# Optimization experiments

Hardware: AMD Instinct MI355X
Metric: run time of the kernel (lower is better)

The kernel has to match this reference:

```python
import jax, jax.numpy as jnp
import numpy as np
from jax import lax
import math

KS = 7  # attention kernel size
PAD = 3


def conv2d(x, w, b, pad):
    y = lax.conv_general_dilated(x, w, (1, 1), [(pad, pad), (pad, pad)],
                                 dimension_numbers=('NCHW', 'OIHW', 'NCHW'))
    return y + b[None, :, None, None]


def unfold(x):
    # x: [B, C, H, W] -> [B, C, KS*KS, H, W], matching nn.Unfold channel-major order
    B, C, H, W = x.shape
    xp = jnp.pad(x, ((0, 0), (0, 0), (PAD, PAD), (PAD, PAD)))
    patches = [xp[:, :, i:i + H, j:j + W] for i in range(KS) for j in range(KS)]
    return jnp.stack(patches, axis=2)


def setup_inputs() -> dict:
    key = jax.random.key(0)
    ks = jax.random.split(key, 12)
    B, H, W = 1, 256, 256
    s = lambda fan: 1.0 / np.sqrt(fan)
    inp = {
        'x': jax.random.normal(ks[0], (B, 6, H, W), jnp.float32),
        'w0': jax.random.normal(ks[1], (48, 3, 3, 3), jnp.float32) * s(3 * 9),
        'b0': jnp.zeros((48,), jnp.float32),
        'w1': jax.random.normal(ks[2], (48, 48, 3, 3), jnp.float32) * s(48 * 9),
        'b1': jnp.zeros((48,), jnp.float32),
        'w2': jax.random.normal(ks[3], (48, 48, 3, 3), jnp.float32) * s(48 * 9),
        'b2': jnp.zeros((48,), jnp.float32),
        'w3': jax.random.normal(ks[4], (24, 48, 3, 3), jnp.float32) * s(48 * 9),
        'b3': jnp.zeros((24,), jnp.float32),
        'skip_w': jax.random.normal(ks[5], (24, 3, 1, 1), jnp.float32) * s(3),
        'skip_b': jnp.zeros((24,), jnp.float32),
        'q_w': jax.random.normal(ks[6], (24, 24, 1, 1), jnp.float32) * s(24),
        'q_b': jnp.zeros((24,), jnp.float32),
        'k_w': jax.random.normal(ks[7], (24, 24, 1, 1), jnp.float32) * s(24),
        'k_b': jnp.zeros((24,), jnp.float32),
        'v_w': jax.random.normal(ks[8], (24, 24, 1, 1), jnp.float32) * s(24),
        'v_b': jnp.zeros((24,), jnp.float32),
    }
    return inp


def reference(x, w0, b0, w1, b1, w2, b2, w3, b3, skip_w, skip_b,
              q_w, q_b, k_w, k_b, v_w, v_b):
    def submodel(t):
        h = jax.nn.relu(conv2d(t, w0, b0, 1))
        h = jax.nn.relu(conv2d(h, w1, b1, 1))
        h = jax.nn.relu(conv2d(h, w2, b2, 1))
        h = jax.nn.relu(conv2d(h, w3, b3, 1))
        return h + conv2d(t, skip_w, skip_b, 0)

    xa, xb = jnp.split(x, 2, axis=1)  # [B,3,H,W] each
    a = submodel(xa)                  # [B,24,H,W]
    b = submodel(xb)

    Q = conv2d(b, q_w, q_b, 0)        # [B,24,H,W]
    K = unfold(conv2d(a, k_w, k_b, 0))  # [B,24,49,H,W]
    V = unfold(conv2d(a, v_w, v_b, 0))  # [B,24,49,H,W]

    C = Q.shape[1]
    A = jnp.einsum('bchw,bcphw->bphw', Q, K) / math.sqrt(C)
    A = jax.nn.softmax(A, axis=1)     # softmax over 49 local positions
    y = jnp.einsum('bphw,bcphw->bchw', A, V)
    return jnp.concatenate([y + a, b], axis=1)  # [B,48,H,W]
```

## Files before the change

kernel.cpp:

```cpp
#include <hip/hip_runtime.h>
#include <math.h>

#define HH 256
#define WW 256
#define NN (HH * WW)

typedef _Float16 f16;
typedef _Float16 f16x8 __attribute__((ext_vector_type(8)));
typedef _Float16 f16x4 __attribute__((ext_vector_type(4)));
typedef float f32x4 __attribute__((ext_vector_type(4)));

#define OQ 75264

__global__ __launch_bounds__(256) void prep_kernel(
    const float* __restrict__ x, const float* __restrict__ w0,
    const float* __restrict__ w1, const float* __restrict__ w2,
    const float* __restrict__ w3, const float* __restrict__ qw,
    const float* __restrict__ kw, const float* __restrict__ vw,
    f16* __restrict__ xh, f16* __restrict__ bf) {
  if (blockIdx.x < 512) {
    int p = blockIdx.x * 256 + threadIdx.x;
    int z = p >= NN;
    int q = p - z * NN;
    const float* xz = x + (size_t)z * 3 * NN;
    f16x4 v;
    v[0] = (f16)xz[q];
    v[1] = (f16)xz[NN + q];
    v[2] = (f16)xz[2 * NN + q];
    v[3] = (f16)0.f;
    *(f16x4*)(xh + (size_t)p * 4) = v;
    return;
  }
  const int O1 = 1536, O2 = O1 + 27648, O3 = O2 + 27648;
  int e = (blockIdx.x - 512) * 256 + threadIdx.x;
  if (e >= OQ + 3072) return;
  float val = 0.f;
  if (e >= OQ) {
    int idx = e - OQ;
    int mat = idx >> 10;
    int r = idx & 1023;
    int nt = r >> 9;
    int lane = (r >> 3) & 63;
    int j = r & 7;
    int n = lane & 15, quad = lane >> 4;
    int ci = quad * 8 + j, co = nt * 16 + n;
    const float* w = (mat == 0) ? qw : (mat == 1) ? kw : vw;
    if (ci < 24 && co < 24) val = w[co * 24 + ci];
  } else if (e < O1) {
    int idx = e;
    int j = idx & 7;
    int lane = (idx >> 3) & 63;
    int nt = idx >> 9;
    int n = lane & 15, quad = lane >> 4;
    int k = quad * 8 + j;
    int cout = nt * 16 + n;
    if (k < 27) {
      int tap = k / 3, ci = k - tap * 3;
      val = w0[(cout * 3 + ci) * 9 + tap];
    }
  } else {
    const float* w;
    int COUT, idx;
    if (e < O2)      { w = w1; COUT = 48; idx = e - O1; }
    else if (e < O3) { w = w2; COUT = 48; idx = e - O2; }
    else             { w = w3; COUT = 24; idx = e - O3; }
    const int NT = (COUT == 48) ? 3 : 2;
    int j = idx & 7;
    int lane = (idx >> 3) & 63;
    int rest = idx >> 9;
    int nt = rest % NT;
    int q2 = rest / NT;
    int kc = q2 & 1;
    int tap = q2 >> 1;
    int n = lane & 15, quad = lane >> 4;
    int ci = kc * 32 + quad * 8 + j;
    int cout = nt * 16 + n;
    if (ci < 48 && cout < COUT) val = w[(cout * 48 + ci) * 9 + tap];
  }
  bf[e] = (f16)val;
}

__global__ __launch_bounds__(256, 2) void conv0_gemm(
    const f16* __restrict__ xh, const f16* __restrict__ bf0,
    const float* __restrict__ bias, f16* __restrict__ outh) {
  extern __shared__ char smem[];
  const int tid = threadIdx.x;
  const int lane = tid & 63, wave = tid >> 6;
  const int n = lane & 15, quad = lane >> 4;
  const int bx = blockIdx.x * 16, by = blockIdx.y * 16, z = blockIdx.z;
  const f16* xz = xh + (size_t)z * NN * 4;

  {
    int p = tid, y = p >> 4, xcol = p & 15;
    int gy = by + y, gx = bx + xcol;
    f16* row = (f16*)(smem + p * 80);
#pragma unroll
    for (int tap = 0; tap < 9; ++tap) {
      int dy = tap / 3, dx = tap - (tap / 3) * 3;
      int sy = gy + dy - 1, sx = gx + dx - 1;
      f16 c0 = (f16)0.f, c1 = c0, c2 = c0;
      if (sy >= 0 && sy < HH && sx >= 0 && sx < WW) {
        const f16* s = xz + ((size_t)sy * WW + sx) * 4;
        c0 = s[0]; c1 = s[1]; c2 = s[2];
      }
      row[tap * 3 + 0] = c0;
      row[tap * 3 + 1] = c1;
      row[tap * 3 + 2] = c2;
    }
#pragma unroll
    for (int k = 27; k < 32; ++k) row[k] = (f16)0.f;
  }
  __syncthreads();

  f32x4 acc[4][3];
#pragma unroll
  for (int nt = 0; nt < 3; ++nt) {
    float bv = bias[nt * 16 + n];
#pragma unroll
    for (int i = 0; i < 4; ++i) acc[i][nt] = (f32x4){bv, bv, bv, bv};
  }
  f16x8 B[3];
#pragma unroll
  for (int nt = 0; nt < 3; ++nt)
    B[nt] = *(const f16x8*)(bf0 + (nt * 64 + lane) * 8);
#pragma unroll
  for (int i = 0; i < 4; ++i) {
    int r = wave * 4 + i;
    f16x8 a = *(const f16x8*)(smem + (r * 16 + n) * 80 + quad * 16);
#pragma unroll
    for (int nt = 0; nt < 3; ++nt)
      acc[i][nt] =
          __builtin_amdgcn_mfma_f32_16x16x32_f16(a, B[nt], acc[i][nt], 0, 0, 0);
  }

  f16* oz = outh + (size_t)z * NN * 48;
#pragma unroll
  for (int i = 0; i < 4; ++i) {
    int y = by + wave * 4 + i;
#pragma unroll
    for (int nt = 0; nt < 3; ++nt)
#pragma unroll
      for (int reg = 0; reg < 4; ++reg)
        oz[((size_t)y * WW + bx + quad * 4 + reg) * 48 + nt * 16 + n] =
            (f16)fmaxf(acc[i][nt][reg], 0.f);
  }
}

template <int NT, int COUT, bool FUSE>
__global__ __launch_bounds__(256, 4) void gemm_conv(
    const f16* __restrict__ in, const f16* __restrict__ bfr,
    const float* __restrict__ bias, f16* __restrict__ outh,
    const float* __restrict__ xsrc, const float* __restrict__ skw,
    const float* __restrict__ skb) {
  extern __shared__ char smem[];
  float* xt = (float*)(smem + 180 * 144);
  const int tid = threadIdx.x;
  const int lane = tid & 63, wave = tid >> 6;
  const int n = lane & 15, quad = lane >> 4;
  const int bx = blockIdx.x * 16, by = blockIdx.y * 8, z = blockIdx.z;
  const f16* inz = in + (size_t)z * NN * 48;

  if (tid < 180) {
    int p = tid;
    int yy = p / 18, xx = p - yy * 18;
    int gy = by + yy - 1, gx = bx + xx - 1;
    float4* dst = (float4*)(smem + p * 144);
    if (gy >= 0 && gy < HH && gx >= 0 && gx < WW) {
      const float4* s = (const float4*)(inz + ((size_t)gy * WW + gx) * 48);
      float4 a0 = s[0], a1 = s[1], a2 = s[2], a3 = s[3], a4 = s[4], a5 = s[5];
      dst[0] = a0; dst[1] = a1; dst[2] = a2;
      dst[3] = a3; dst[4] = a4; dst[5] = a5;
      dst[6] = make_float4(0, 0, 0, 0);
      dst[7] = make_float4(0, 0, 0, 0);
    } else {
      float4 zz = make_float4(0, 0, 0, 0);
#pragma unroll
      for (int c = 0; c < 8; ++c) dst[c] = zz;
    }
  }
  if (FUSE) {
    for (int i = tid; i < 384; i += 256) {
      int c = i >> 7, p = i & 127;
      xt[i] = xsrc[(size_t)z * 3 * NN + c * NN + (by + (p >> 4)) * WW + bx +
                   (p & 15)];
    }
  }
  __syncthreads();

  f32x4 acc[2][NT];
#pragma unroll
  for (int nt = 0; nt < NT; ++nt) {
    int cc = nt * 16 + n;
    float bv = (cc < COUT) ? bias[cc] : 0.f;
#pragma unroll
    for (int i = 0; i < 2; ++i) acc[i][nt] = (f32x4){bv, bv, bv, bv};
  }

  const int r0 = wave * 2;
#pragma unroll 1
  for (int tap = 0; tap < 9; ++tap) {
    const int dy = tap / 3, dx = tap - dy * 3;
    f16x8 B[2][NT];
#pragma unroll
    for (int kc = 0; kc < 2; ++kc)
#pragma unroll
      for (int nt = 0; nt < NT; ++nt)
        B[kc][nt] = *(const f16x8*)(bfr +
                                    (((tap * 2 + kc) * NT + nt) * 64 + lane) * 8);
#pragma unroll
    for (int i = 0; i < 2; ++i) {
      const int p = (r0 + i + dy) * 18 + (n + dx);
      const char* ap = smem + p * 144;
      f16x8 a0 = *(const f16x8*)(ap + quad * 16);
      f16x8 a1 = *(const f16x8*)(ap + 64 + quad * 16);
#pragma unroll
      for (int nt = 0; nt < NT; ++nt)
        acc[i][nt] = __builtin_amdgcn_mfma_f32_16x16x32_f16(a0, B[0][nt],
                                                            acc[i][nt], 0, 0, 0);
#pragma unroll
      for (int nt = 0; nt < NT; ++nt)
        acc[i][nt] = __builtin_amdgcn_mfma_f32_16x16x32_f16(a1, B[1][nt],
                                                            acc[i][nt], 0, 0, 0);
    }
  }

  if (!FUSE) {
    f16* oz = outh + (size_t)z * NN * 48;
#pragma unroll
    for (int i = 0; i < 2; ++i) {
      int y = by + r0 + i;
#pragma unroll
      for (int nt = 0; nt < NT; ++nt)
#pragma unroll
        for (int reg = 0; reg < 4; ++reg)
          oz[((size_t)y * WW + bx + quad * 4 + reg) * 48 + nt * 16 + n] =
              (f16)fmaxf(acc[i][nt][reg], 0.f);
    }
  } else {
    f16* oz = outh + (size_t)z * NN * 32;
#pragma unroll
    for (int i = 0; i < 2; ++i) {
      int y = by + r0 + i;
#pragma unroll
      for (int nt = 0; nt < NT; ++nt) {
        int cc = nt * 16 + n;
        float s0 = 0.f, s1 = 0.f, s2 = 0.f, sb0 = 0.f;
        if (cc < 24) {
          s0 = skw[cc * 3 + 0];
          s1 = skw[cc * 3 + 1];
          s2 = skw[cc * 3 + 2];
          sb0 = skb[cc];
        }
#pragma unroll
        for (int reg = 0; reg < 4; ++reg) {
          float v = 0.f;
          if (cc < 24) {
            int pl = (r0 + i) * 16 + quad * 4 + reg;
            float sk = sb0 + s0 * xt[pl] + s1 * xt[128 + pl] + s2 * xt[256 + pl];
            v = fmaxf(acc[i][nt][reg], 0.f) + sk;
          }
          oz[((size_t)(y * WW + bx + quad * 4 + reg)) * 32 + cc] = (f16)v;
        }
      }
    }
  }
}

__global__ __launch_bounds__(256) void q_mfma(const f16* __restrict__ ABh,
                                              const f16* __restrict__ bf,
                                              const float* __restrict__ qb,
                                              f16* __restrict__ Qh) {
  const int tid = threadIdx.x;
  const int lane = tid & 63, wave = tid >> 6;
  const int n = lane & 15, quad = lane >> 4;
  const f16* src = ABh + (size_t)NN * 32;
  f16x8 QF[2];
#pragma unroll
  for (int nt = 0; nt < 2; ++nt)
    QF[nt] = *(const f16x8*)(bf + OQ + (nt * 64 + lane) * 8);
  float qbias[2];
#pragma unroll
  for (int nt = 0; nt < 2; ++nt) {
    int cc = nt * 16 + n;
    qbias[nt] = (cc < 24) ? qb[cc] : 0.f;
  }
#pragma unroll
  for (int t = 0; t < 4; ++t) {
    int T = blockIdx.x * 16 + wave * 4 + t;
    size_t p0 = (size_t)T * 16;
    f16x8 a8 = *(const f16x8*)(src + p0 * 32 + n * 32 + quad * 8);
#pragma unroll
    for (int nt = 0; nt < 2; ++nt) {
      f32x4 acc = {qbias[nt], qbias[nt], qbias[nt], qbias[nt]};
      acc = __builtin_amdgcn_mfma_f32_16x16x32_f16(a8, QF[nt], acc, 0, 0, 0);
      int cc = nt * 16 + n;
      if (cc < 24) {
#pragma unroll
        for (int reg = 0; reg < 4; ++reg)
          Qh[(p0 + quad * 4 + reg) * 24 + cc] = (f16)acc[reg];
      }
    }
  }
}

__device__ inline float dot8p(f16x8 a, f16x8 b, float acc) {
#if __has_builtin(__builtin_amdgcn_fdot2)
  acc = __builtin_amdgcn_fdot2(__builtin_shufflevector(a, a, 0, 1),
                               __builtin_shufflevector(b, b, 0, 1), acc, false);
  acc = __builtin_amdgcn_fdot2(__builtin_shufflevector(a, a, 2, 3),
                               __builtin_shufflevector(b, b, 2, 3), acc, false);
  acc = __builtin_amdgcn_fdot2(__builtin_shufflevector(a, a, 4, 5),
                               __builtin_shufflevector(b, b, 4, 5), acc, false);
  acc = __builtin_amdgcn_fdot2(__builtin_shufflevector(a, a, 6, 7),
                               __builtin_shufflevector(b, b, 6, 7), acc, false);
  return acc;
#else
#pragma unroll
  for (int i = 0; i < 8; ++i) acc += (float)a[i] * (float)b[i];
  return acc;
#endif
}

__global__ __launch_bounds__(256, 3) void attn_kernel(
    const f16* __restrict__ Qh, const f16* __restrict__ ABh,
    const f16* __restrict__ bf, const float* __restrict__ kb,
    const float* __restrict__ vb, float* __restrict__ out) {
  extern __shared__ f16 kv[];
  const int tid = threadIdx.x;
  const int lane = tid & 63, wave = tid >> 6;
  const int n16 = lane & 15, quad = lane >> 4;
  const int bx = blockIdx.x * 32, by = blockIdx.y * 8;
  const int xl = tid & 31, yl = tid >> 5;
  const int p = (by + yl) * WW + bx + xl;
  const f16* ah = ABh;
  const f16* bh = ABh + (size_t)NN * 32;

  f16x8 q0 = *(const f16x8*)(Qh + (size_t)p * 24);
  f16x8 q1 = *(const f16x8*)(Qh + (size_t)p * 24 + 8);
  f16x8 q2 = *(const f16x8*)(Qh + (size_t)p * 24 + 16);

  for (int idx = tid; idx < 2128; idx += 256) {
    int row = idx / 152;
    int rem = idx - row * 152;
    int pxl = rem >> 2;
    int c = rem & 3;
    int gy = by + row - 3, gx = bx + pxl - 3;
    f16x8 v = {};
    if (gy >= 0 && gy < HH && gx >= 0 && gx < WW)
      v = *(const f16x8*)(ah + ((size_t)(gy * WW + gx)) * 32 + c * 8);
    *(f16x8*)(kv + (row * 38 + pxl) * 56 + c * 8) = v;
  }
  __syncthreads();

  const f16* cs = kv + ((yl + 3) * 38 + xl + 3) * 56;
  f16x8 a0 = *(const f16x8*)(cs);
  f16x8 a1 = *(const f16x8*)(cs + 8);
  f16x8 a2 = *(const f16x8*)(cs + 16);
  __syncthreads();

  {
    f16x8 KF[2], VF[2];
#pragma unroll
    for (int nt = 0; nt < 2; ++nt) {
      KF[nt] = *(const f16x8*)(bf + OQ + 1024 + (nt * 64 + lane) * 8);
      VF[nt] = *(const f16x8*)(bf + OQ + 2048 + (nt * 64 + lane) * 8);
    }
    float kbias[2], vbias[2];
#pragma unroll
    for (int nt = 0; nt < 2; ++nt) {
      int cc = nt * 16 + n16;
      kbias[nt] = (cc < 24) ? kb[cc] : 0.f;
      vbias[nt] = (cc < 24) ? vb[cc] : 0.f;
    }
    for (int t = wave; t < 34; t += 4) {
      f16x8 a8 = *(const f16x8*)(kv + (t * 16 + n16) * 56 + quad * 8);
#pragma unroll
      for (int nt = 0; nt < 2; ++nt) {
        f32x4 ak = {kbias[nt], kbias[nt], kbias[nt], kbias[nt]};
        f32x4 av = {vbias[nt], vbias[nt], vbias[nt], vbias[nt]};
        ak = __builtin_amdgcn_mfma_f32_16x16x32_f16(a8, KF[nt], ak, 0, 0, 0);
        av = __builtin_amdgcn_mfma_f32_16x16x32_f16(a8, VF[nt], av, 0, 0, 0);
        int cc = nt * 16 + n16;
        if (cc < 24) {
#pragma unroll
          for (int reg = 0; reg < 4; ++reg) {
            f16* slot = kv + (t * 16 + quad * 4 + reg) * 56;
            slot[cc] = (f16)ak[reg];
            slot[24 + cc] = (f16)av[reg];
          }
        }
      }
    }
  }
  __syncthreads();

  float s[49];
#pragma unroll
  for (int pp = 0; pp < 49; ++pp) {
    int dy = pp / 7, dx = pp - dy * 7;
    const f16* base = kv + ((yl + dy) * 38 + xl + dx) * 56;
    f16x8 k0 = *(const f16x8*)(base);
    f16x8 k1 = *(const f16x8*)(base + 8);
    f16x8 k2 = *(const f16x8*)(base + 16);
    float d = 0.f;
    d = dot8p(q0, k0, d);
    d = dot8p(q1, k1, d);
    d = dot8p(q2, k2, d);
    s[pp] = d * 0.20412414523193154f;
  }

  float m = s[0];
#pragma unroll
  for (int pp = 1; pp < 49; ++pp) m = fmaxf(m, s[pp]);
  float den = 0.f;
#pragma unroll
  for (int pp = 0; pp < 49; ++pp) {
    float e = __expf(s[pp] - m);
    s[pp] = e;
    den += e;
  }
  const float inv = 1.f / den;

  f16x8 y0 = {}, y1 = {}, y2 = {};
#pragma unroll
  for (int pp = 0; pp < 49; ++pp) {
    int dy = pp / 7, dx = pp - dy * 7;
    const f16* base = kv + ((yl + dy) * 38 + xl + dx) * 56 + 24;
    f16 wh = (f16)(s[pp] * inv);
    f16x8 w8 = {wh, wh, wh, wh, wh, wh, wh, wh};
    f16x8 v0 = *(const f16x8*)(base);
    f16x8 v1 = *(const f16x8*)(base + 8);
    f16x8 v2 = *(const f16x8*)(base + 16);
    y0 = v0 * w8 + y0;
    y1 = v1 * w8 + y1;
    y2 = v2 * w8 + y2;
  }

  f16x8 b0 = *(const f16x8*)(bh + (size_t)p * 32);
  f16x8 b1 = *(const f16x8*)(bh + (size_t)p * 32 + 8);
  f16x8 b2 = *(const f16x8*)(bh + (size_t)p * 32 + 16);
#pragma unroll
  for (int c = 0; c < 8; ++c) {
    out[(size_t)c * NN + p] = (float)y0[c] + (float)a0[c];
    out[(size_t)(8 + c) * NN + p] = (float)y1[c] + (float)a1[c];
    out[(size_t)(16 + c) * NN + p] = (float)y2[c] + (float)a2[c];
    out[(size_t)(24 + c) * NN + p] = (float)b0[c];
    out[(size_t)(32 + c) * NN + p] = (float)b1[c];
    out[(size_t)(40 + c) * NN + p] = (float)b2[c];
  }
}

extern "C" void kernel_launch(void* const* d_in, const int* in_sizes, int n_in,
                              void* d_out, int out_size, void* d_ws,
                              size_t ws_size, hipStream_t stream) {
  const float* x = (const float*)d_in[0];
  const float* w0 = (const float*)d_in[1];
  const float* b0 = (const float*)d_in[2];
  const float* w1 = (const float*)d_in[3];
  const float* b1 = (const float*)d_in[4];
  const float* w2 = (const float*)d_in[5];
  const float* b2 = (const float*)d_in[6];
  const float* w3 = (const float*)d_in[7];
  const float* b3 = (const float*)d_in[8];
  const float* sw = (const float*)d_in[9];
  const float* sb = (const float*)d_in[10];
  const float* qw = (const float*)d_in[11];
  const float* qb = (const float*)d_in[12];
  const float* kw = (const float*)d_in[13];
  const float* kb = (const float*)d_in[14];
  const float* vw = (const float*)d_in[15];
  const float* vb = (const float*)d_in[16];
  float* out = (float*)d_out;
  float* ws = (float*)d_ws;

  f16* Qh = (f16*)(ws);
  f16* ABh = (f16*)(ws + (size_t)12 * NN);
  f16* ACT0 = (f16*)(ws + (size_t)44 * NN);
  f16* ACT1 = (f16*)(ws + (size_t)92 * NN);
  f16* XH = (f16*)(ws + (size_t)140 * NN);
  f16* BF = (f16*)(ws + (size_t)144 * NN);

  prep_kernel<<<dim3(818), dim3(256), 0, stream>>>(x, w0, w1, w2, w3, qw, kw,
                                                   vw, XH, BF);

  conv0_gemm<<<dim3(16, 16, 2), dim3(256), 256 * 80, stream>>>(XH, BF, b0,
                                                               ACT0);
  dim3 g2(16, 32, 2);
  gemm_conv<3, 48, false><<<g2, dim3(256), 180 * 144, stream>>>(
      ACT0, BF + 1536, b1, ACT1, nullptr, nullptr, nullptr);
  gemm_conv<3, 48, false><<<g2, dim3(256), 180 * 144, stream>>>(
      ACT1, BF + 29184, b2, ACT0, nullptr, nullptr, nullptr);
  gemm_conv<2, 24, true><<<g2, dim3(256), 180 * 144 + 1536, stream>>>(
      ACT0, BF + 56832, b3, ABh, x, sw, sb);

  q_mfma<<<dim3(256), dim3(256), 0, stream>>>(ABh, BF, qb, Qh);

  attn_kernel<<<dim3(8, 32), dim3(256), 544 * 112, stream>>>(Qh, ABh, BF, kb,
                                                             vb, out);
}
```

Before: 158.8 us.

## Fuse whole pipeline into one cooperative persistent kernel with grid syncs

Replaces the seven separate kernel launches with a single cooperative kernel of 512 blocks that runs weight repacking, the four conv layers, Q projection and local attention as phases separated by grid-wide syncs. Conv0 now reads fp32 input directly, which drops the separate fp16 input conversion pass. The attention phase computes K/V projections per tile in shared memory and splits the 49 neighbours across two thread halves, merging them with an online-softmax combine. The aim is to remove launch gaps and inter-kernel idle time. The cost is fixed grid size, grid.sync overhead, and a smaller attention tile that recomputes K/V over a larger halo, which may lower per-phase efficiency.

Measured after the change: 480.6 us. 203% more time.

```diff
diff --git a/kernel.cpp b/kernel.cpp
--- a/kernel.cpp
+++ b/kernel.cpp
@@ -1,16 +1,486 @@
 #include <hip/hip_runtime.h>
+#include <hip/hip_cooperative_groups.h>
 #include <math.h>
+
+namespace cg = cooperative_groups;
 
 #define HH 256
 #define WW 256
 #define NN (HH * WW)
 
 typedef _Float16 f16;
+typedef _Float16 f16x4 __attribute__((ext_vector_type(4)));
 typedef _Float16 f16x8 __attribute__((ext_vector_type(8)));
-typedef _Float16 f16x4 __attribute__((ext_vector_type(4)));
 typedef float f32x4 __attribute__((ext_vector_type(4)));
 
 #define OQ 75264
+
+__device__ inline float dot8p(f16x8 a, f16x8 b, float acc) {
+#if __has_builtin(__builtin_amdgcn_fdot2)
+  acc = __builtin_amdgcn_fdot2(__builtin_shufflevector(a, a, 0, 1),
+                               __builtin_shufflevector(b, b, 0, 1), acc, false);
+  acc = __builtin_amdgcn_fdot2(__builtin_shufflevector(a, a, 2, 3),
+                               __builtin_shufflevector(b, b, 2, 3), acc, false);
+  acc = __builtin_amdgcn_fdot2(__builtin_shufflevector(a, a, 4, 5),
+                               __builtin_shufflevector(b, b, 4, 5), acc, false);
+  acc = __builtin_amdgcn_fdot2(__builtin_shufflevector(a, a, 6, 7),
+                               __builtin_shufflevector(b, b, 6, 7), acc, false);
+  return acc;
+#else
+#pragma unroll
+  for (int i = 0; i < 8; ++i) acc += (float)a[i] * (float)b[i];
+  return acc;
+#endif
+}
+
+__device__ __forceinline__ float repack_elem(
+    int e, const float* __restrict__ w0, const float* __restrict__ w1,
+    const float* __restrict__ w2, const float* __restrict__ w3,
+    const float* __restrict__ qw, const float* __restrict__ kw,
+    const float* __restrict__ vw) {
+  const int O1 = 1536, O2 = O1 + 27648, O3 = O2 + 27648;
+  float val = 0.f;
+  if (e >= OQ) {
+    int idx = e - OQ;
+    int mat = idx >> 10;
+    int r = idx & 1023;
+    int nt = r >> 9;
+    int ln = (r >> 3) & 63;
+    int j = r & 7;
+    int nn = ln & 15, qd = ln >> 4;
+    int ci = qd * 8 + j, co = nt * 16 + nn;
+    const float* w = (mat == 0) ? qw : (mat == 1) ? kw : vw;
+    if (ci < 24 && co < 24) val = w[co * 24 + ci];
+  } else if (e < O1) {
+    int j = e & 7;
+    int ln = (e >> 3) & 63;
+    int nt = e >> 9;
+    int nn = ln & 15, qd = ln >> 4;
+    int k = qd * 8 + j;
+    int cout = nt * 16 + nn;
+    if (k < 27) {
+      int tap = k / 3, ci = k - tap * 3;
+      val = w0[(cout * 3 + ci) * 9 + tap];
+    }
+  } else {
+    const float* w;
+    int COUT, idx;
+    if (e < O2)      { w = w1; COUT = 48; idx = e - O1; }
+    else if (e < O3) { w = w2; COUT = 48; idx = e - O2; }
+    else             { w = w3; COUT = 24; idx = e - O3; }
+    const int NT = (COUT == 48) ? 3 : 2;
+    int j = idx & 7;
+    int ln = (idx >> 3) & 63;
+    int rest = idx >> 9;
+    int nt = rest % NT;
+    int q2 = rest / NT;
+    int kc = q2 & 1;
+    int tap = q2 >> 1;
+    int nn = ln & 15, qd = ln >> 4;
+    int ci = kc * 32 + qd * 8 + j;
+    int cout = nt * 16 + nn;
+    if (ci < 48 && cout < COUT) val = w[(cout * 48 + ci) * 9 + tap];
+  }
+  return val;
+}
+
+template <int NT, int COUT, bool FUSE>
+__device__ __forceinline__ void conv_layer(
+    const f16* __restrict__ in, const f16* __restrict__ bfr,
+    const float* __restrict__ bias, f16* __restrict__ outh,
+    const float* __restrict__ xsrc, const float* __restrict__ skw,
+    const float* __restrict__ skb, char* smem, int tid, int bx, int by,
+    int z) {
+  float* xt = (float*)(smem + 180 * 144);
+  const int lane = tid & 63, wave = tid >> 6;
+  const int n = lane & 15, quad = lane >> 4;
+  const f16* inz = in + (size_t)z * NN * 48;
+
+  if (tid < 180) {
+    int p = tid;
+    int yy = p / 18, xx = p - yy * 18;
+    int gy = by + yy - 1, gx = bx + xx - 1;
+    float4* dst = (float4*)(smem + p * 144);
+    if (gy >= 0 && gy < HH && gx >= 0 && gx < WW) {
+      const float4* s = (const float4*)(inz + ((size_t)gy * WW + gx) * 48);
+      float4 a0 = s[0], a1 = s[1], a2 = s[2], a3 = s[3], a4 = s[4], a5 = s[5];
+      dst[0] = a0; dst[1] = a1; dst[2] = a2;
+      dst[3] = a3; dst[4] = a4; dst[5] = a5;
+      dst[6] = make_float4(0, 0, 0, 0);
+      dst[7] = make_float4(0, 0, 0, 0);
+    } else {
+      float4 zz = make_float4(0, 0, 0, 0);
+#pragma unroll
+      for (int c = 0; c < 8; ++c) dst[c] = zz;
+    }
+  }
+  if (FUSE) {
+    for (int i = tid; i < 384; i += 256) {
+      int c = i >> 7, p = i & 127;
+      xt[i] = xsrc[(size_t)z * 3 * NN + c * NN + (by + (p >> 4)) * WW + bx +
+                   (p & 15)];
+    }
+  }
+  __syncthreads();
+
+  f32x4 acc[2][NT];
+#pragma unroll
+  for (int nt = 0; nt < NT; ++nt) {
+    int cc = nt * 16 + n;
+    float bv = (cc < COUT) ? bias[cc] : 0.f;
+#pragma unroll
+    for (int i = 0; i < 2; ++i) acc[i][nt] = (f32x4){bv, bv, bv, bv};
+  }
+
+  const int r0 = wave * 2;
+#pragma unroll 1
+  for (int tap = 0; tap < 9; ++tap) {
+    const int dy = tap / 3, dx = tap - dy * 3;
+    f16x8 B[2][NT];
+#pragma unroll
+    for (int kc = 0; kc < 2; ++kc)
+#pragma unroll
+      for (int nt = 0; nt < NT; ++nt)
+        B[kc][nt] = *(const f16x8*)(bfr +
+                                    (((tap * 2 + kc) * NT + nt) * 64 + lane) * 8);
+#pragma unroll
+    for (int i = 0; i < 2; ++i) {
+      const int p = (r0 + i + dy) * 18 + (n + dx);
+      const char* ap = smem + p * 144;
+      f16x8 a0 = *(const f16x8*)(ap + quad * 16);
+      f16x8 a1 = *(const f16x8*)(ap + 64 + quad * 16);
+#pragma unroll
+      for (int nt = 0; nt < NT; ++nt)
+        acc[i][nt] = __builtin_amdgcn_mfma_f32_16x16x32_f16(a0, B[0][nt],
+                                                            acc[i][nt], 0, 0, 0);
+#pragma unroll
+      for (int nt = 0; nt < NT; ++nt)
+        acc[i][nt] = __builtin_amdgcn_mfma_f32_16x16x32_f16(a1, B[1][nt],
+                                                            acc[i][nt], 0, 0, 0);
+    }
+  }
+
+  if (!FUSE) {
+    f16* oz = outh + (size_t)z * NN * 48;
+#pragma unroll
+    for (int i = 0; i < 2; ++i) {
+      int y = by + r0 + i;
+#pragma unroll
+      for (int nt = 0; nt < NT; ++nt)
+#pragma unroll
+        for (int reg = 0; reg < 4; ++reg)
+          oz[((size_t)y * WW + bx + quad * 4 + reg) * 48 + nt * 16 + n] =
+              (f16)fmaxf(acc[i][nt][reg], 0.f);
+    }
+  } else {
+    f16* oz = outh + (size_t)z * NN * 32;
+#pragma unroll
+    for (int i = 0; i < 2; ++i) {
+      int y = by + r0 + i;
+#pragma unroll
+      for (int nt = 0; nt < NT; ++nt) {
+        int cc = nt * 16 + n;
+        float s0 = 0.f, s1 = 0.f, s2 = 0.f, sbv = 0.f;
+        if (cc < 24) {
+          s0 = skw[cc * 3 + 0];
+          s1 = skw[cc * 3 + 1];
+          s2 = skw[cc * 3 + 2];
+          sbv = skb[cc];
+        }
+#pragma unroll
+        for (int reg = 0; reg < 4; ++reg) {
+          float v = 0.f;
+          if (cc < 24) {
+            int pl = (r0 + i) * 16 + quad * 4 + reg;
+            float sk = sbv + s0 * xt[pl] + s1 * xt[128 + pl] + s2 * xt[256 + pl];
+            v = fmaxf(acc[i][nt][reg], 0.f) + sk;
+          }
+          oz[((size_t)(y * WW + bx + quad * 4 + reg)) * 32 + cc] = (f16)v;
+        }
+      }
+    }
+  }
+  __syncthreads();
+}
+
+__global__ __launch_bounds__(256, 4) void mega(
+    const float* __restrict__ x, const float* __restrict__ w0,
+    const float* __restrict__ b0, const float* __restrict__ w1,
+    const float* __restrict__ b1, const float* __restrict__ w2,
+    const float* __restrict__ b2, const float* __restrict__ w3,
+    const float* __restrict__ b3, const float* __restrict__ sw,
+    const float* __restrict__ sb, const float* __restrict__ qw,
+    const float* __restrict__ qb, const float* __restrict__ kw,
+    const float* __restrict__ kb, const float* __restrict__ vw,
+    const float* __restrict__ vb, float* __restrict__ out,
+    f16* __restrict__ ACT0, f16* __restrict__ ACT1, f16* __restrict__ ABh,
+    f16* __restrict__ BF) {
+  extern __shared__ char smem[];
+  cg::grid_group grid = cg::this_grid();
+  const int tid = threadIdx.x;
+  const int bz = blockIdx.x;
+  const int lane = tid & 63, wave = tid >> 6;
+  const int n = lane & 15, quad = lane >> 4;
+
+  if (bz < 306) {
+    int e = bz * 256 + tid;
+    BF[e] = (f16)repack_elem(e, w0, w1, w2, w3, qw, kw, vw);
+  }
+  grid.sync();
+
+#pragma unroll 1
+  for (int job = bz; job < 1024; job += 512) {
+    const int z = job >> 9, tt = job & 511;
+    const int bx = (tt & 15) * 16, by = (tt >> 4) * 8;
+    if (tid < 128) {
+      int yy = tid >> 4, xc = tid & 15;
+      int gy = by + yy, gx = bx + xc;
+      const float* xz = x + (size_t)z * 3 * NN;
+      f16* row = (f16*)(smem + tid * 80);
+#pragma unroll
+      for (int tap = 0; tap < 9; ++tap) {
+        int dy = tap / 3, dx = tap - (tap / 3) * 3;
+        int sy = gy + dy - 1, sx = gx + dx - 1;
+        f16 c0 = (f16)0.f, c1 = c0, c2 = c0;
+        if (sy >= 0 && sy < HH && sx >= 0 && sx < WW) {
+          int o = sy * WW + sx;
+          c0 = (f16)xz[o];
+          c1 = (f16)xz[NN + o];
+          c2 = (f16)xz[2 * NN + o];
+        }
+        row[tap * 3 + 0] = c0;
+        row[tap * 3 + 1] = c1;
+        row[tap * 3 + 2] = c2;
+      }
+#pragma unroll
+      for (int k = 27; k < 32; ++k) row[k] = (f16)0.f;
+    }
+    __syncthreads();
+
+    f16x8 B0[3];
+#pragma unroll
+    for (int nt = 0; nt < 3; ++nt)
+      B0[nt] = *(const f16x8*)(BF + (nt * 64 + lane) * 8);
+    f16* oz = ACT0 + (size_t)z * NN * 48;
+#pragma unroll
+    for (int u = 0; u < 2; ++u) {
+      int T = wave * 2 + u;
+      f16x8 a = *(const f16x8*)(smem + (T * 16 + n) * 80 + quad * 16);
+#pragma unroll
+      for (int nt = 0; nt < 3; ++nt) {
+        float bv = b0[nt * 16 + n];
+        f32x4 acc = {bv, bv, bv, bv};
+        acc = __builtin_amdgcn_mfma_f32_16x16x32_f16(a, B0[nt], acc, 0, 0, 0);
+        int gy = by + T;
+#pragma unroll
+        for (int reg = 0; reg < 4; ++reg)
+          oz[((size_t)gy * WW + bx + quad * 4 + reg) * 48 + nt * 16 + n] =
+              (f16)fmaxf(acc[reg], 0.f);
+      }
+    }
+    __syncthreads();
+  }
+  grid.sync();
+
+#pragma unroll 1
+  for (int job = bz; job < 1024; job += 512) {
+    const int z = job >> 9, tt = job & 511;
+    conv_layer<3, 48, false>(ACT0, BF + 1536, b1, ACT1, nullptr, nullptr,
+                             nullptr, smem, tid, (tt & 15) * 16, (tt >> 4) * 8,
+                             z);
+  }
+  grid.sync();
+#pragma unroll 1
+  for (int job = bz; job < 1024; job += 512) {
+    const int z = job >> 9, tt = job & 511;
+    conv_layer<3, 48, false>(ACT1, BF + 29184, b2, ACT0, nullptr, nullptr,
+                             nullptr, smem, tid, (tt & 15) * 16, (tt >> 4) * 8,
+                             z);
+  }
+  grid.sync();
+#pragma unroll 1
+  for (int job = bz; job < 1024; job += 512) {
+    const int z = job >> 9, tt = job & 511;
+    conv_layer<2, 24, true>(ACT0, BF + 56832, b3, ABh, x, sw, sb, smem, tid,
+                            (tt & 15) * 16, (tt >> 4) * 8, z);
+  }
+  grid.sync();
+
+  {
+    f16* kv = (f16*)smem;
+    f16* Wq = (f16*)(smem + 35840);
+    float* Qbv = (float*)(smem + 35840 + 1152);
+    const int bxA = (bz & 15) * 16, byA = (bz >> 4) * 8;
+
+    for (int i = tid; i < 576; i += 256) Wq[i] = (f16)qw[i];
+    if (tid < 24) Qbv[tid] = qb[tid];
+
+    for (int idx = tid; idx < 1232; idx += 256) {
+      int slot = idx >> 2, c = idx & 3;
+      int row = slot / 22, pxl = slot - row * 22;
+      int gy = byA + row - 3, gx = bxA + pxl - 3;
+      f16x8 v = {};
+      if (gy >= 0 && gy < HH && gx >= 0 && gx < WW)
+        v = *(const f16x8*)(ABh + ((size_t)(gy * WW + gx)) * 32 + c * 8);
+      *(f16x8*)(kv + slot * 56 + c * 8) = v;
+    }
+    __syncthreads();
+
+    const int t7 = tid & 127, half = tid >> 7;
+    const int yl = t7 >> 4, xl = t7 & 15;
+    const int pg = (byA + yl) * WW + bxA + xl;
+
+    const f16* cs = kv + ((yl + 3) * 22 + (xl + 3)) * 56;
+    f16x8 a0 = *(const f16x8*)(cs);
+    f16x8 a1 = *(const f16x8*)(cs + 8);
+    f16x8 a2 = *(const f16x8*)(cs + 16);
+
+    const f16* bhp = ABh + (size_t)NN * 32 + (size_t)pg * 32;
+    f16x8 bb0 = *(const f16x8*)(bhp);
+    f16x8 bb1 = *(const f16x8*)(bhp + 8);
+    f16x8 bb2 = *(const f16x8*)(bhp + 16);
+    float qf[24];
+#pragma unroll
+    for (int co = 0; co < 24; ++co) {
+      float acc = Qbv[co];
+      acc = dot8p(bb0, *(const f16x8*)(Wq + co * 24), acc);
+      acc = dot8p(bb1, *(const f16x8*)(Wq + co * 24 + 8), acc);
+      acc = dot8p(bb2, *(const f16x8*)(Wq + co * 24 + 16), acc);
+      qf[co] = acc;
+    }
+    f16x8 q0, q1, q2;
+#pragma unroll
+    for (int c = 0; c < 8; ++c) {
+      q0[c] = (f16)qf[c];
+      q1[c] = (f16)qf[8 + c];
+      q2[c] = (f16)qf[16 + c];
+    }
+    __syncthreads();
+
+    {
+      f16x8 KF[2], VF[2];
+#pragma unroll
+      for (int nt = 0; nt < 2; ++nt) {
+        KF[nt] = *(const f16x8*)(BF + OQ + 1024 + (nt * 64 + lane) * 8);
+        VF[nt] = *(const f16x8*)(BF + OQ + 2048 + (nt * 64 + lane) * 8);
+      }
+      float kbias[2], vbias[2];
+#pragma unroll
+      for (int nt = 0; nt < 2; ++nt) {
+        int cc = nt * 16 + n;
+        kbias[nt] = (cc < 24) ? kb[cc] : 0.f;
+        vbias[nt] = (cc < 24) ? vb[cc] : 0.f;
+      }
+      for (int t = wave; t < 20; t += 4) {
+        f16x8 a8 = *(const f16x8*)(kv + (t * 16 + n) * 56 + quad * 8);
+#pragma unroll
+        for (int nt = 0; nt < 2; ++nt) {
+          f32x4 ak = {kbias[nt], kbias[nt], kbias[nt], kbias[nt]};
+          f32x4 av = {vbias[nt], vbias[nt], vbias[nt], vbias[nt]};
+          ak = __builtin_amdgcn_mfma_f32_16x16x32_f16(a8, KF[nt], ak, 0, 0, 0);
+          av = __builtin_amdgcn_mfma_f32_16x16x32_f16(a8, VF[nt], av, 0, 0, 0);
+          int cc = nt * 16 + n;
+          if (cc < 24) {
+#pragma unroll
+            for (int reg = 0; reg < 4; ++reg) {
+              f16* slot = kv + (t * 16 + quad * 4 + reg) * 56;
+              slot[cc] = (f16)ak[reg];
+              slot[24 + cc] = (f16)av[reg];
+            }
+          }
+        }
+      }
+    }
+    __syncthreads();
+
+    float s[25];
+    float m = -3e38f;
+#pragma unroll
+    for (int i = 0; i < 25; ++i) {
+      int pp = half * 25 + i;
+      if (pp < 49) {
+        int dy = pp / 7, dx = pp - (pp / 7) * 7;
+        const f16* base = kv + ((yl + dy) * 22 + (xl + dx)) * 56;
+        f16x8 k0 = *(const f16x8*)(base);
+        f16x8 k1 = *(const f16x8*)(base + 8);
+        f16x8 k2 = *(const f16x8*)(base + 16);
+        float d = 0.f;
+        d = dot8p(q0, k0, d);
+        d = dot8p(q1, k1, d);
+        d = dot8p(q2, k2, d);
+        s[i] = d * 0.20412414523193154f;
+        m = fmaxf(m, s[i]);
+      } else {
+        s[i] = -3e38f;
+      }
+    }
+    float den = 0.f;
+#pragma unroll
+    for (int i = 0; i < 25; ++i) {
+      float e = __expf(s[i] - m);
+      s[i] = e;
+      den += e;
+    }
+
+    f16x8 y0 = {}, y1 = {}, y2 = {};
+#pragma unroll
+    for (int i = 0; i < 25; ++i) {
+      int pp = half * 25 + i;
+      if (pp < 49) {
+        int dy = pp / 7, dx = pp - (pp / 7) * 7;
+        const f16* base = kv + ((yl + dy) * 22 + (xl + dx)) * 56 + 24;
+        f16 wh = (f16)s[i];
+        f16x8 w8 = {wh, wh, wh, wh, wh, wh, wh, wh};
+        f16x8 v0 = *(const f16x8*)(base);
+        f16x8 v1 = *(const f16x8*)(base + 8);
+        f16x8 v2 = *(const f16x8*)(base + 16);
+        y0 = v0 * w8 + y0;
+        y1 = v1 * w8 + y1;
+        y2 = v2 * w8 + y2;
+      }
+    }
+    __syncthreads();
+
+    if (half == 1) {
+      f16* ex = kv + t7 * 56;
+      *(f16x8*)(ex) = y0;
+      *(f16x8*)(ex + 8) = y1;
+      *(f16x8*)(ex + 16) = y2;
+      float* mf = (float*)(ex + 24);
+      mf[0] = m;
+      mf[1] = den;
+    }
+    __syncthreads();
+
+    if (half == 0) {
+      const f16* ex = kv + t7 * 56;
+      f16x8 yb0 = *(const f16x8*)(ex);
+      f16x8 yb1 = *(const f16x8*)(ex + 8);
+      f16x8 yb2 = *(const f16x8*)(ex + 16);
+      const float* mf = (const float*)(ex + 24);
+      float mB = mf[0], dB = mf[1];
+      float M = fmaxf(m, mB);
+      float fa = __expf(m - M), fb = __expf(mB - M);
+      float inv = 1.f / (den * fa + dB * fb);
+#pragma unroll
+      for (int c = 0; c < 8; ++c) {
+        out[(size_t)c * NN + pg] =
+            ((float)y0[c] * fa + (float)yb0[c] * fb) * inv + (float)a0[c];
+        out[(size_t)(8 + c) * NN + pg] =
+            ((float)y1[c] * fa + (float)yb1[c] * fb) * inv + (float)a1[c];
+        out[(size_t)(16 + c) * NN + pg] =
+            ((float)y2[c] * fa + (float)yb2[c] * fb) * inv + (float)a2[c];
+      }
+    } else {
+#pragma unroll
+      for (int c = 0; c < 8; ++c) {
+        out[(size_t)(24 + c) * NN + pg] = (float)bb0[c];
+        out[(size_t)(32 + c) * NN + pg] = (float)bb1[c];
+        out[(size_t)(40 + c) * NN + pg] = (float)bb2[c];
+      }
+    }
+  }
+}
 
 __global__ __launch_bounds__(256) void prep_kernel(
     const float* __restrict__ x, const float* __restrict__ w0,
@@ -31,53 +501,9 @@
     *(f16x4*)(xh + (size_t)p * 4) = v;
     return;
   }
-  const int O1 = 1536, O2 = O1 + 27648, O3 = O2 + 27648;
   int e = (blockIdx.x - 512) * 256 + threadIdx.x;
   if (e >= OQ + 3072) return;
-  float val = 0.f;
-  if (e >= OQ) {
-    int idx = e - OQ;
-    int mat = idx >> 10;
-    int r = idx & 1023;
-    int nt = r >> 9;
-    int lane = (r >> 3) & 63;
-    int j = r & 7;
-    int n = lane & 15, quad = lane >> 4;
-    int ci = quad * 8 + j, co = nt * 16 + n;
-    const float* w = (mat == 0) ? qw : (mat == 1) ? kw : vw;
-    if (ci < 24 && co < 24) val = w[co * 24 + ci];
-  } else if (e < O1) {
-    int idx = e;
-    int j = idx & 7;
-    int lane = (idx >> 3) & 63;
-    int nt = idx >> 9;
-    int n = lane & 15, quad = lane >> 4;
-    int k = quad * 8 + j;
-    int cout = nt * 16 + n;
-    if (k < 27) {
-      int tap = k / 3, ci = k - tap * 3;
-      val = w0[(cout * 3 + ci) * 9 + tap];
-    }
-  } else {
-    const float* w;
-    int COUT, idx;
-    if (e < O2)      { w = w1; COUT = 48; idx = e - O1; }
-    else if (e < O3) { w = w2; COUT = 48; idx = e - O2; }
-    else             { w = w3; COUT = 24; idx = e - O3; }
-    const int NT = (COUT == 48) ? 3 : 2;
-    int j = idx & 7;
-    int lane = (idx >> 3) & 63;
-    int rest = idx >> 9;
-    int nt = rest % NT;
-    int q2 = rest / NT;
-    int kc = q2 & 1;
-    int tap = q2 >> 1;
-    int n = lane & 15, quad = lane >> 4;
-    int ci = kc * 32 + quad * 8 + j;
-    int cout = nt * 16 + n;
-    if (ci < 48 && cout < COUT) val = w[(cout * 48 + ci) * 9 + tap];
-  }
-  bf[e] = (f16)val;
+  bf[e] = (f16)repack_elem(e, w0, w1, w2, w3, qw, kw, vw);
 }
 
 __global__ __launch_bounds__(256, 2) void conv0_gemm(
@@ -153,117 +579,9 @@
     const float* __restrict__ xsrc, const float* __restrict__ skw,
     const float* __restrict__ skb) {
   extern __shared__ char smem[];
-  float* xt = (float*)(smem + 180 * 144);
-  const int tid = threadIdx.x;
-  const int lane = tid & 63, wave = tid >> 6;
-  const int n = lane & 15, quad = lane >> 4;
-  const int bx = blockIdx.x * 16, by = blockIdx.y * 8, z = blockIdx.z;
-  const f16* inz = in + (size_t)z * NN * 48;
-
-  if (tid < 180) {
-    int p = tid;
-    int yy = p / 18, xx = p - yy * 18;
-    int gy = by + yy - 1, gx = bx + xx - 1;
-    float4* dst = (float4*)(smem + p * 144);
-    if (gy >= 0 && gy < HH && gx >= 0 && gx < WW) {
-      const float4* s = (const float4*)(inz + ((size_t)gy * WW + gx) * 48);
-      float4 a0 = s[0], a1 = s[1], a2 = s[2], a3 = s[3], a4 = s[4], a5 = s[5];
-      dst[0] = a0; dst[1] = a1; dst[2] = a2;
-      dst[3] = a3; dst[4] = a4; dst[5] = a5;
-      dst[6] = make_float4(0, 0, 0, 0);
-      dst[7] = make_float4(0, 0, 0, 0);
-    } else {
-      float4 zz = make_float4(0, 0, 0, 0);
-#pragma unroll
-      for (int c = 0; c < 8; ++c) dst[c] = zz;
-    }
-  }
-  if (FUSE) {
-    for (int i = tid; i < 384; i += 256) {
-      int c = i >> 7, p = i & 127;
-      xt[i] = xsrc[(size_t)z * 3 * NN + c * NN + (by + (p >> 4)) * WW + bx +
-                   (p & 15)];
-    }
-  }
-  __syncthreads();
-
-  f32x4 acc[2][NT];
-#pragma unroll
-  for (int nt = 0; nt < NT; ++nt) {
-    int cc = nt * 16 + n;
-    float bv = (cc < COUT) ? bias[cc] : 0.f;
-#pragma unroll
-    for (int i = 0; i < 2; ++i) acc[i][nt] = (f32x4){bv, bv, bv, bv};
-  }
-
-  const int r0 = wave * 2;
-#pragma unroll 1
-  for (int tap = 0; tap < 9; ++tap) {
-    const int dy = tap / 3, dx = tap - dy * 3;
-    f16x8 B[2][NT];
-#pragma unroll
-    for (int kc = 0; kc < 2; ++kc)
-#pragma unroll
-      for (int nt = 0; nt < NT; ++nt)
-        B[kc][nt] = *(const f16x8*)(bfr +
-                                    (((tap * 2 + kc) * NT + nt) * 64 + lane) * 8);
-#pragma unroll
-    for (int i = 0; i < 2; ++i) {
-      const int p = (r0 + i + dy) * 18 + (n + dx);
-      const char* ap = smem + p * 144;
-      f16x8 a0 = *(const f16x8*)(ap + quad * 16);
-      f16x8 a1 = *(const f16x8*)(ap + 64 + quad * 16);
-#pragma unroll
-      for (int nt = 0; nt < NT; ++nt)
-        acc[i][nt] = __builtin_amdgcn_mfma_f32_16x16x32_f16(a0, B[0][nt],
-                                                            acc[i][nt], 0, 0, 0);
-#pragma unroll
-      for (int nt = 0; nt < NT; ++nt)
-        acc[i][nt] = __builtin_amdgcn_mfma_f32_16x16x32_f16(a1, B[1][nt],
-                                                            acc[i][nt], 0, 0, 0);
-    }
-  }
-
-  if (!FUSE) {
-    f16* oz = outh + (size_t)z * NN * 48;
-#pragma unroll
-    for (int i = 0; i < 2; ++i) {
-      int y = by + r0 + i;
-#pragma unroll
-      for (int nt = 0; nt < NT; ++nt)
-#pragma unroll
-        for (int reg = 0; reg < 4; ++reg)
-          oz[((size_t)y * WW + bx + quad * 4 + reg) * 48 + nt * 16 + n] =
-              (f16)fmaxf(acc[i][nt][reg], 0.f);
-    }
-  } else {
-    f16* oz = outh + (size_t)z * NN * 32;
-#pragma unroll
-    for (int i = 0; i < 2; ++i) {
-      int y = by + r0 + i;
-#pragma unroll
-      for (int nt = 0; nt < NT; ++nt) {
-        int cc = nt * 16 + n;
-        float s0 = 0.f, s1 = 0.f, s2 = 0.f, sb0 = 0.f;
-        if (cc < 24) {
-          s0 = skw[cc * 3 + 0];
-          s1 = skw[cc * 3 + 1];
-          s2 = skw[cc * 3 + 2];
-          sb0 = skb[cc];
-        }
-#pragma unroll
-        for (int reg = 0; reg < 4; ++reg) {
-          float v = 0.f;
-          if (cc < 24) {
-            int pl = (r0 + i) * 16 + quad * 4 + reg;
-            float sk = sb0 + s0 * xt[pl] + s1 * xt[128 + pl] + s2 * xt[256 + pl];
-            v = fmaxf(acc[i][nt][reg], 0.f) + sk;
-          }
-          oz[((size_t)(y * WW + bx + quad * 4 + reg)) * 32 + cc] = (f16)v;
-        }
-      }
-    }
-  }
+  conv_layer<NT, COUT, FUSE>(in, bfr, bias, outh, xsrc, skw, skb, smem,
+                             threadIdx.x, blockIdx.x * 16, blockIdx.y * 8,
+                             blockIdx.z);
 }
 
 __global__ __launch_bounds__(256) void q_mfma(const f16* __restrict__ ABh,
@@ -301,24 +619,6 @@
       }
     }
   }
-}
-
-__device__ inline float dot8p(f16x8 a, f16x8 b, float acc) {
-#if __has_builtin(__builtin_amdgcn_fdot2)
-  acc = __builtin_amdgcn_fdot2(__builtin_shufflevector(a, a, 0, 1),
-                               __builtin_shufflevector(b, b, 0, 1), acc, false);
-  acc = __builtin_amdgcn_fdot2(__builtin_shufflevector(a, a, 2, 3),
-                               __builtin_shufflevector(b, b, 2, 3), acc, false);
-  acc = __builtin_amdgcn_fdot2(__builtin_shufflevector(a, a, 4, 5),
-                               __builtin_shufflevector(b, b, 4, 5), acc, false);
-  acc = __builtin_amdgcn_fdot2(__builtin_shufflevector(a, a, 6, 7),
-                               __builtin_shufflevector(b, b, 6, 7), acc, false);
-  return acc;
-#else
-#pragma unroll
-  for (int i = 0; i < 8; ++i) acc += (float)a[i] * (float)b[i];
-  return acc;
-#endif
 }
 
 __global__ __launch_bounds__(256, 3) void attn_kernel(
@@ -471,30 +771,45 @@
   const float* vw = (const float*)d_in[15];
   const float* vb = (const float*)d_in[16];
   float* out = (float*)d_out;
-  float* ws = (float*)d_ws;
-
-  f16* Qh = (f16*)(ws);
-  f16* ABh = (f16*)(ws + (size_t)12 * NN);
-  f16* ACT0 = (f16*)(ws + (size_t)44 * NN);
-  f16* ACT1 = (f16*)(ws + (size_t)92 * NN);
-  f16* XH = (f16*)(ws + (size_t)140 * NN);
-  f16* BF = (f16*)(ws + (size_t)144 * NN);
-
-  prep_kernel<<<dim3(818), dim3(256), 0, stream>>>(x, w0, w1, w2, w3, qw, kw,
-                                                   vw, XH, BF);
-
-  conv0_gemm<<<dim3(16, 16, 2), dim3(256), 256 * 80, stream>>>(XH, BF, b0,
-                                                               ACT0);
-  dim3 g2(16, 32, 2);
-  gemm_conv<3, 48, false><<<g2, dim3(256), 180 * 144, stream>>>(
-      ACT0, BF + 1536, b1, ACT1, nullptr, nullptr, nullptr);
-  gemm_conv<3, 48, false><<<g2, dim3(256), 180 * 144, stream>>>(
-      ACT1, BF + 29184, b2, ACT0, nullptr, nullptr, nullptr);
-  gemm_conv<2, 24, true><<<g2, dim3(256), 180 * 144 + 1536, stream>>>(
-      ACT0, BF + 56832, b3, ABh, x, sw, sb);
-
-  q_mfma<<<dim3(256), dim3(256), 0, stream>>>(ABh, BF, qb, Qh);
-
-  attn_kernel<<<dim3(8, 32), dim3(256), 544 * 112, stream>>>(Qh, ABh, BF, kb,
-                                                             vb, out);
-}
+
+  f16* base = (f16*)d_ws;
+  f16* ACT0 = base;
+  f16* ACT1 = base + (size_t)96 * NN;
+  f16* ABh = base + (size_t)192 * NN;
+  f16* Qh = base + (size_t)256 * NN;
+  f16* BF = base + (size_t)280 * NN;
+  f16* XH = base + (size_t)282 * NN;
+
+  int dev = 0;
+  hipGetDevice(&dev);
+  int coop = 0;
+  hipDeviceGetAttribute(&coop, hipDeviceAttributeCooperativeLaunch, dev);
+
+  bool launched = false;
+  if (coop) {
+    void* args[] = {&x,  &w0, &b0, &w1, &b1, &w2, &b2,  &w3,   &b3,
+                    &sw, &sb, &qw, &qb, &kw, &kb, &vw,  &vb,   &out,
+                    &ACT0, &ACT1, &ABh, &BF};
+    hipError_t err = hipLaunchCooperativeKernel((void*)mega, dim3(512),
+                                                dim3(256), args, 37088, stream);
+    launched = (err == hipSuccess);
+    if (!launched) (void)hipGetLastError();
+  }
+
+  if (!launched) {
+    prep_kernel<<<dim3(818), dim3(256), 0, stream>>>(x, w0, w1, w2, w3, qw, kw,
+                                                     vw, XH, BF);
+    conv0_gemm<<<dim3(16, 16, 2), dim3(256), 256 * 80, stream>>>(XH, BF, b0,
+                                                                 ACT0);
+    dim3 g2(16, 32, 2);
+    gemm_conv<3, 48, false><<<g2, dim3(256), 180 * 144, stream>>>(
+        ACT0, BF + 1536, b1, ACT1, nullptr, nullptr, nullptr);
+    gemm_conv<3, 48, false><<<g2, dim3(256), 180 * 144, stream>>>(
+        ACT1, BF + 29184, b2, ACT0, nullptr, nullptr, nullptr);
+    gemm_conv<2, 24, true><<<g2, dim3(256), 180 * 144 + 1536, stream>>>(
+        ACT0, BF + 56832, b3, ABh, x, sw, sb);
+    q_mfma<<<dim3(256), dim3(256), 0, stream>>>(ABh, BF, qb, Qh);
+    attn_kernel<<<dim3(8, 32), dim3(256), 544 * 112, stream>>>(Qh, ABh, BF, kb,
+                                                               vb, out);
+  }
+}
```
